# Performance work log

Measured on AMD Instinct MI355X. Metric: run time of the kernel, lower is better.

## Reference

```python
import jax, jax.numpy as jnp
import numpy as np

N = 100000
E = 3200000
K = 10
ALPHA = 0.1
EPS = 1e-5


def setup_inputs() -> dict:
    key = jax.random.key(0)
    ks = jax.random.split(key, 12)
    x = jax.random.normal(ks[0], (N, 512), dtype=jnp.float32)
    edge_index = jax.random.randint(ks[1], (2, E), 0, N, dtype=jnp.int32)
    w1 = jax.random.normal(ks[2], (128, 512), dtype=jnp.float32) * 0.02
    b1 = jnp.zeros((128,), jnp.float32)
    g1 = jnp.ones((128,), jnp.float32)
    be1 = jnp.zeros((128,), jnp.float32)
    m1 = jax.random.normal(ks[3], (128,), dtype=jnp.float32) * 0.1
    v1 = jax.random.uniform(ks[4], (128,), dtype=jnp.float32, minval=0.5, maxval=1.5)
    w2 = jax.random.normal(ks[5], (128, 128), dtype=jnp.float32) * 0.02
    b2 = jnp.zeros((128,), jnp.float32)
    g2 = jnp.ones((128,), jnp.float32)
    be2 = jnp.zeros((128,), jnp.float32)
    m2 = jax.random.normal(ks[6], (128,), dtype=jnp.float32) * 0.1
    v2 = jax.random.uniform(ks[7], (128,), dtype=jnp.float32, minval=0.5, maxval=1.5)
    w3 = jax.random.normal(ks[8], (3, 128), dtype=jnp.float32) * 0.02
    b3 = jnp.zeros((3,), jnp.float32)
    return dict(x=x, edge_index=edge_index, w1=w1, b1=b1, g1=g1, be1=be1, m1=m1, v1=v1,
                w2=w2, b2=b2, g2=g2, be2=be2, m2=m2, v2=v2, w3=w3, b3=b3)


def _bn(y, g, be, m, v):
    return (y - m) * jax.lax.rsqrt(v + EPS) * g + be


def reference(x, edge_index, w1, b1, g1, be1, m1, v1, w2, b2, g2, be2, m2, v2, w3, b3):
    # MLP (eval mode: BN uses running stats, dropout is identity)
    h = jax.nn.relu(_bn(x @ w1.T + b1, g1, be1, m1, v1))
    h = h + jax.nn.relu(_bn(h @ w2.T + b2, g2, be2, m2, v2))
    h = h @ w3.T + b3  # [N, 3]

    # APPNP propagation with GCN normalization + self-loops
    loop = jnp.arange(N, dtype=edge_index.dtype)
    src = jnp.concatenate([edge_index[0], loop])
    dst = jnp.concatenate([edge_index[1], loop])
    deg = jax.ops.segment_sum(jnp.ones_like(src, dtype=h.dtype), dst, num_segments=N)
    dinv = jnp.where(deg > 0, jax.lax.rsqrt(deg), 0.0)
    norm = dinv[src] * dinv[dst]  # [E+N]

    h0 = h
    z = h
    for _ in range(K):
        msg = z[src] * norm[:, None]
        z = jax.ops.segment_sum(msg, dst, num_segments=N)
        z = (1.0 - ALPHA) * z + ALPHA * h0
    return jax.nn.log_softmax(z, axis=1)
```

## Files before the change

kernel.cpp:

```cpp
#include <hip/hip_runtime.h>
#include <cstdint>
#include <cstddef>

#define N_NODES 100000
#define D_IN 512
#define ALPHA 0.1f
#define EPS_BN 1e-5f
#define M_TILE 128
#define BK 64

#define CBITS 8
#define CNODES 256
#define NCBIN 391
#define TILE 8192
#define EPT 32
#define BINCAP 9216

typedef float f32x4 __attribute__((ext_vector_type(4)));
typedef __bf16 bf16x8 __attribute__((ext_vector_type(8)));
typedef unsigned short u16x8 __attribute__((ext_vector_type(8)));
typedef unsigned short u16x4 __attribute__((ext_vector_type(4)));

__device__ __forceinline__ unsigned short f2bf(float f) {
  unsigned u = __float_as_uint(f);
  u += 0x7fffu + ((u >> 16) & 1u);
  return (unsigned short)(u >> 16);
}
__device__ __forceinline__ float bf2f(unsigned short h) {
  return __uint_as_float(((unsigned)h) << 16);
}

__global__ void k_prep(const float* __restrict__ w1, const float* __restrict__ b1,
                       const float* __restrict__ g1, const float* __restrict__ be1,
                       const float* __restrict__ m1, const float* __restrict__ v1,
                       const float* __restrict__ w2, const float* __restrict__ b2,
                       const float* __restrict__ g2, const float* __restrict__ be2,
                       const float* __restrict__ m2, const float* __restrict__ v2,
                       unsigned short* __restrict__ w1b, unsigned short* __restrict__ w2b,
                       float* __restrict__ bias1, float* __restrict__ bias2,
                       int* __restrict__ bincur) {
  int idx = blockIdx.x * 256 + threadIdx.x;
  if (idx < 65536) {
    int n = idx >> 9;
    float s = g1[n] * rsqrtf(v1[n] + EPS_BN);
    w1b[idx] = f2bf(w1[idx] * s);
  } else if (idx < 81920) {
    int i = idx - 65536;
    int n = i >> 7;
    float s = g2[n] * rsqrtf(v2[n] + EPS_BN);
    w2b[i] = f2bf(w2[i] * s);
  } else if (idx < 82048) {
    int c = idx - 81920;
    float s = g1[c] * rsqrtf(v1[c] + EPS_BN);
    bias1[c] = (b1[c] - m1[c]) * s + be1[c];
  } else if (idx < 82176) {
    int c = idx - 82048;
    float s = g2[c] * rsqrtf(v2[c] + EPS_BN);
    bias2[c] = (b2[c] - m2[c]) * s + be2[c];
  }
  int bi = idx - 82176;
  if (bi >= 0 && bi < NCBIN) bincur[bi] = 0;
}

__global__ void k_scan1(const int* __restrict__ deg, int* __restrict__ bsum) {
  __shared__ int red[256];
  int t = threadIdx.x;
  int i = blockIdx.x * 256 + t;
  red[t] = (i < N_NODES) ? deg[i] : 0;
  __syncthreads();
  for (int off = 128; off > 0; off >>= 1) {
    if (t < off) red[t] += red[t + off];
    __syncthreads();
  }
  if (t == 0) bsum[blockIdx.x] = red[0];
}

#define NB_SCAN 391
__global__ void k_scan2(int* __restrict__ bsum) {
  __shared__ int s[448];
  int t = threadIdx.x;
  for (int i = t; i < 448; i += 256) s[i] = (i < NB_SCAN) ? bsum[i] : 0;
  __syncthreads();
  if (t < 64) {
    int base = t * 7;
    int vals[7];
    int sum = 0;
#pragma unroll
    for (int j = 0; j < 7; ++j) { vals[j] = s[base + j]; sum += vals[j]; }
    int x = sum;
#pragma unroll
    for (int off = 1; off < 64; off <<= 1) {
      int y = __shfl_up(x, off, 64);
      if (t >= off) x += y;
    }
    int run = x - sum;
#pragma unroll
    for (int j = 0; j < 7; ++j) { int tmp = vals[j]; s[base + j] = run; run += tmp; }
  }
  __syncthreads();
  for (int i = t; i < NB_SCAN; i += 256) bsum[i] = s[i];
}

__global__ void k_scan3(const int* __restrict__ deg, const int* __restrict__ bsum,
                        int* __restrict__ row_start, float* __restrict__ dinv, int E) {
  __shared__ int sb[2][256];
  int t = threadIdx.x;
  int i = blockIdx.x * 256 + t;
  int d = (i < N_NODES) ? deg[i] : 0;
  sb[0][t] = d;
  __syncthreads();
  int cur = 0;
#pragma unroll
  for (int off = 1; off < 256; off <<= 1) {
    int val = sb[cur][t] + ((t >= off) ? sb[cur][t - off] : 0);
    sb[cur ^ 1][t] = val;
    __syncthreads();
    cur ^= 1;
  }
  int incl = sb[cur][t];
  int ex = incl - d;
  if (i < N_NODES) {
    int rs = bsum[blockIdx.x] + ex;
    row_start[i] = rs;
    dinv[i] = rsqrtf((float)(d + 1));
  }
  if (i == N_NODES) row_start[N_NODES] = E;
}

__global__ __launch_bounds__(256) void k_binA(const int* __restrict__ src,
                                              const int* __restrict__ dst, int E,
                                              int* __restrict__ bincur,
                                              unsigned* __restrict__ binned) {
  __shared__ unsigned stage[TILE];
  __shared__ int cnt[NCBIN];
  __shared__ int loff[NCBIN + 1];
  __shared__ int goff[NCBIN];
  __shared__ int sc[2][256];
  const int tid = threadIdx.x;

  for (int i = tid; i < NCBIN; i += 256) cnt[i] = 0;
  __syncthreads();

  const int e0 = blockIdx.x * TILE;
  const int n = min(TILE, E - e0);

  unsigned pk[EPT];
  int bp[EPT];
#pragma unroll
  for (int i = 0; i < EPT; ++i) {
    int o = i * 256 + tid;
    if (o < n) {
      int e = e0 + o;
      int d = dst[e];
      int s = src[e];
      int b = d >> CBITS;
      pk[i] = (unsigned)s | ((unsigned)(d & (CNODES - 1)) << 17);
      int p = atomicAdd(&cnt[b], 1);
      bp[i] = b | (p << 9);
    } else bp[i] = -1;
  }
  __syncthreads();

  int c0 = (2 * tid     < NCBIN) ? cnt[2 * tid]     : 0;
  int c1 = (2 * tid + 1 < NCBIN) ? cnt[2 * tid + 1] : 0;
  sc[0][tid] = c0 + c1;
  __syncthreads();
  int cur = 0;
#pragma unroll
  for (int off = 1; off < 256; off <<= 1) {
    sc[cur ^ 1][tid] = sc[cur][tid] + ((tid >= off) ? sc[cur][tid - off] : 0);
    __syncthreads();
    cur ^= 1;
  }
  int ex = sc[cur][tid] - (c0 + c1);
  if (2 * tid < NCBIN) loff[2 * tid] = ex;
  if (2 * tid + 1 < NCBIN) loff[2 * tid + 1] = ex + c0;
  if (tid == 255) loff[NCBIN] = sc[cur][255];
  __syncthreads();
  for (int i = tid; i < NCBIN; i += 256)
    if (cnt[i] > 0) goff[i] = atomicAdd(&bincur[i], cnt[i]);
  __syncthreads();

#pragma unroll
  for (int i = 0; i < EPT; ++i) {
    if (bp[i] >= 0) {
      int b = bp[i] & 511;
      int p = bp[i] >> 9;
      stage[loff[b] + p] = pk[i];
    }
  }
  __syncthreads();

  for (int i = tid; i < n; i += 256) {
    int lo = 0, hi = NCBIN;
    while (hi - lo > 1) { int mid = (lo + hi) >> 1; if (loff[mid] <= i) lo = mid; else hi = mid; }
    int b = lo;
    binned[(size_t)b * BINCAP + goff[b] + (i - loff[b])] = stage[i];
  }
}

__global__ __launch_bounds__(256) void k_binB1(const unsigned* __restrict__ binned,
                                               const int* __restrict__ bincur,
                                               int* __restrict__ deg) {
  __shared__ int lcnt[CNODES];
  int b = blockIdx.x;
  int t = threadIdx.x;
  lcnt[t] = 0;
  __syncthreads();
  int cnt = bincur[b];
  const unsigned* bp = binned + (size_t)b * BINCAP;
  for (int i = t; i < cnt; i += 256) {
    unsigned v = bp[i];
    atomicAdd(&lcnt[v >> 17], 1);
  }
  __syncthreads();
  int node = (b << CBITS) + t;
  if (node < N_NODES) deg[node] = lcnt[t];
}

__global__ __launch_bounds__(256) void k_binB2(const unsigned* __restrict__ binned,
                                               const int* __restrict__ bincur,
                                               const int* __restrict__ row_start,
                                               unsigned* __restrict__ csr_col) {
  __shared__ unsigned sortbuf[BINCAP];
  __shared__ int lcur[CNODES];
  int b = blockIdx.x;
  int t = threadIdx.x;
  int node0 = b << CBITS;
  int nodes = min(CNODES, N_NODES - node0);
  int rs0 = row_start[node0];
  if (t < nodes) lcur[t] = row_start[node0 + t] - rs0;
  __syncthreads();
  int cnt = bincur[b];
  const unsigned* bp = binned + (size_t)b * BINCAP;
  for (int i = t; i < cnt; i += 256) {
    unsigned v = bp[i];
    int p = atomicAdd(&lcur[v >> 17], 1);
    sortbuf[p] = v & 0x1FFFFu;
  }
  __syncthreads();
  for (int i = t; i < cnt; i += 256) csr_col[rs0 + i] = sortbuf[i];
}

__global__ __launch_bounds__(256, 2) void k_mlp(
    const float* __restrict__ x, const unsigned short* __restrict__ w1b,
    const unsigned short* __restrict__ w2b, const float* __restrict__ bias1,
    const float* __restrict__ bias2, const float* __restrict__ w3,
    const float* __restrict__ b3, const float* __restrict__ dinv,
    float4* __restrict__ h0, float4* __restrict__ zt) {
  __shared__ unsigned short arena[35840];
  __shared__ float lds_w3[384];
  unsigned short* lds_x = arena;
  unsigned short* lds_w = arena + 9216;
  unsigned short* lds_h = arena;
  unsigned short* lds_w2 = arena + 18432;

  const int tid = threadIdx.x;
  const int lane = tid & 63;
  const int wv = tid >> 6;
  const int fr = lane & 15;
  const int kq = (lane >> 4) * 8;
  const int rq = (lane >> 4) * 4;
  const int row0 = blockIdx.x * M_TILE;

  for (int i = tid; i < 384; i += 256) lds_w3[i] = w3[i];

#pragma unroll
  for (int it = 0; it < 8; ++it) {
    int idx = it * 256 + tid;
    int n = idx >> 4, c8 = idx & 15;
    uint4 v = *(const uint4*)(w2b + n * 128 + c8 * 8);
    *(uint4*)(lds_w2 + n * 136 + c8 * 8) = v;
  }

  f32x4 zero4 = {0.f, 0.f, 0.f, 0.f};
  f32x4 acc[2][8];
#pragma unroll
  for (int mt = 0; mt < 2; ++mt)
#pragma unroll
    for (int nt = 0; nt < 8; ++nt) acc[mt][nt] = zero4;

  for (int kb = 0; kb < D_IN; kb += BK) {
#pragma unroll
    for (int it = 0; it < 8; ++it) {
      int idx = it * 256 + tid;
      int r = idx >> 4, c4 = idx & 15;
      int gm = row0 + r;
      if (gm >= N_NODES) gm = N_NODES - 1;
      float4 v = *(const float4*)(x + (size_t)gm * D_IN + kb + c4 * 4);
      u16x4 o;
      o.x = f2bf(v.x); o.y = f2bf(v.y); o.z = f2bf(v.z); o.w = f2bf(v.w);
      *(u16x4*)(lds_x + r * 72 + c4 * 4) = o;
    }
#pragma unroll
    for (int it = 0; it < 4; ++it) {
      int idx = it * 256 + tid;
      int n = idx >> 3, c8 = idx & 7;
      uint4 v = *(const uint4*)(w1b + n * 512 + kb + c8 * 8);
      *(uint4*)(lds_w + n * 72 + c8 * 8) = v;
    }
    __syncthreads();
#pragma unroll
    for (int kk = 0; kk < BK; kk += 32) {
      bf16x8 a[2], b[8];
#pragma unroll
      for (int mt = 0; mt < 2; ++mt)
        a[mt] = __builtin_bit_cast(bf16x8, *(const u16x8*)(lds_x + (wv * 32 + mt * 16 + fr) * 72 + kk + kq));
#pragma unroll
      for (int nt = 0; nt < 8; ++nt)
        b[nt] = __builtin_bit_cast(bf16x8, *(const u16x8*)(lds_w + (nt * 16 + fr) * 72 + kk + kq));
#pragma unroll
      for (int mt = 0; mt < 2; ++mt)
#pragma unroll
        for (int nt = 0; nt < 8; ++nt)
          acc[mt][nt] = __builtin_amdgcn_mfma_f32_16x16x32_bf16(a[mt], b[nt], acc[mt][nt], 0, 0, 0);
    }
    __syncthreads();
  }

  float b1v[8], b2v[8];
#pragma unroll
  for (int nt = 0; nt < 8; ++nt) {
    b1v[nt] = bias1[nt * 16 + fr];
    b2v[nt] = bias2[nt * 16 + fr];
  }
  float hr[2][8][4];
#pragma unroll
  for (int mt = 0; mt < 2; ++mt)
#pragma unroll
    for (int nt = 0; nt < 8; ++nt)
#pragma unroll
      for (int r = 0; r < 4; ++r) {
        int rl = wv * 32 + mt * 16 + rq + r;
        int cl = nt * 16 + fr;
        float h = acc[mt][nt][r] + b1v[nt];
        h = h > 0.f ? h : 0.f;
        hr[mt][nt][r] = h;
        lds_h[rl * 136 + cl] = f2bf(h);
      }
  __syncthreads();

  f32x4 acc2[2][8];
#pragma unroll
  for (int mt = 0; mt < 2; ++mt)
#pragma unroll
    for (int nt = 0; nt < 8; ++nt) acc2[mt][nt] = zero4;
#pragma unroll
  for (int kk = 0; kk < 128; kk += 32) {
    bf16x8 a[2], b[8];
#pragma unroll
    for (int mt = 0; mt < 2; ++mt)
      a[mt] = __builtin_bit_cast(bf16x8, *(const u16x8*)(lds_h + (wv * 32 + mt * 16 + fr) * 136 + kk + kq));
#pragma unroll
    for (int nt = 0; nt < 8; ++nt)
      b[nt] = __builtin_bit_cast(bf16x8, *(const u16x8*)(lds_w2 + (nt * 16 + fr) * 136 + kk + kq));
#pragma unroll
    for (int mt = 0; mt < 2; ++mt)
#pragma unroll
      for (int nt = 0; nt < 8; ++nt)
        acc2[mt][nt] = __builtin_amdgcn_mfma_f32_16x16x32_bf16(a[mt], b[nt], acc2[mt][nt], 0, 0, 0);
  }
  __syncthreads();

#pragma unroll
  for (int mt = 0; mt < 2; ++mt)
#pragma unroll
    for (int nt = 0; nt < 8; ++nt)
#pragma unroll
      for (int r = 0; r < 4; ++r) {
        int rl = wv * 32 + mt * 16 + rq + r;
        int cl = nt * 16 + fr;
        float t2 = acc2[mt][nt][r] + b2v[nt];
        t2 = t2 > 0.f ? t2 : 0.f;
        lds_h[rl * 136 + cl] = f2bf(hr[mt][nt][r] + t2);
      }
  __syncthreads();

  if (tid < 128) {
    int m = tid;
    int gm = row0 + m;
    if (gm < N_NODES) {
      float a0 = 0.f, a1 = 0.f, a2 = 0.f;
#pragma unroll 8
      for (int c = 0; c < 128; ++c) {
        float hv = bf2f(lds_h[m * 136 + c]);
        a0 += hv * lds_w3[c];
        a1 += hv * lds_w3[128 + c];
        a2 += hv * lds_w3[256 + c];
      }
      float z0 = a0 + b3[0], z1 = a1 + b3[1], z2 = a2 + b3[2];
      float di = dinv[gm];
      h0[gm] = make_float4(z0, z1, z2, 0.f);
      zt[gm] = make_float4(di * z0, di * z1, di * z2, 0.f);
    }
  }
}

__global__ void k_iter(const float4* __restrict__ ztin, float4* __restrict__ ztout,
                       const int* __restrict__ row_start, const unsigned* __restrict__ csr_col,
                       const float* __restrict__ dinv, const float4* __restrict__ h0) {
  int i = blockIdx.x * 256 + threadIdx.x;
  if (i >= N_NODES) return;
  float4 self = ztin[i];
  float sx = self.x, sy = self.y, sz = self.z;
  int r0 = row_start[i], r1 = row_start[i + 1];
  int j = r0;
  for (; j + 1 < r1; j += 2) {
    int c0 = csr_col[j], c1 = csr_col[j + 1];
    float4 v0 = ztin[c0];
    float4 v1 = ztin[c1];
    sx += v0.x + v1.x; sy += v0.y + v1.y; sz += v0.z + v1.z;
  }
  if (j < r1) {
    float4 v = ztin[csr_col[j]];
    sx += v.x; sy += v.y; sz += v.z;
  }
  float di = dinv[i];
  float4 h = h0[i];
  float zx = (1.f - ALPHA) * di * sx + ALPHA * h.x;
  float zy = (1.f - ALPHA) * di * sy + ALPHA * h.y;
  float zz = (1.f - ALPHA) * di * sz + ALPHA * h.z;
  ztout[i] = make_float4(di * zx, di * zy, di * zz, 0.f);
}

__global__ void k_final(const float4* __restrict__ ztin,
                        const int* __restrict__ row_start, const unsigned* __restrict__ csr_col,
                        const float* __restrict__ dinv, const float4* __restrict__ h0,
                        float* __restrict__ out) {
  int i = blockIdx.x * 256 + threadIdx.x;
  if (i >= N_NODES) return;
  float4 self = ztin[i];
  float sx = self.x, sy = self.y, sz = self.z;
  int r0 = row_start[i], r1 = row_start[i + 1];
  int j = r0;
  for (; j + 1 < r1; j += 2) {
    int c0 = csr_col[j], c1 = csr_col[j + 1];
    float4 v0 = ztin[c0];
    float4 v1 = ztin[c1];
    sx += v0.x + v1.x; sy += v0.y + v1.y; sz += v0.z + v1.z;
  }
  if (j < r1) {
    float4 v = ztin[csr_col[j]];
    sx += v.x; sy += v.y; sz += v.z;
  }
  float di = dinv[i];
  float4 h = h0[i];
  float zx = (1.f - ALPHA) * di * sx + ALPHA * h.x;
  float zy = (1.f - ALPHA) * di * sy + ALPHA * h.y;
  float zz = (1.f - ALPHA) * di * sz + ALPHA * h.z;
  float mx = fmaxf(zx, fmaxf(zy, zz));
  float l = logf(expf(zx - mx) + expf(zy - mx) + expf(zz - mx));
  out[i * 3 + 0] = zx - mx - l;
  out[i * 3 + 1] = zy - mx - l;
  out[i * 3 + 2] = zz - mx - l;
}

extern "C" void kernel_launch(void* const* d_in, const int* in_sizes, int n_in,
                              void* d_out, int out_size, void* d_ws, size_t ws_size,
                              hipStream_t stream) {
  const float* x   = (const float*)d_in[0];
  const int*   ei  = (const int*)d_in[1];
  const float* w1  = (const float*)d_in[2];
  const float* b1  = (const float*)d_in[3];
  const float* g1  = (const float*)d_in[4];
  const float* be1 = (const float*)d_in[5];
  const float* m1  = (const float*)d_in[6];
  const float* v1  = (const float*)d_in[7];
  const float* w2  = (const float*)d_in[8];
  const float* b2  = (const float*)d_in[9];
  const float* g2  = (const float*)d_in[10];
  const float* be2 = (const float*)d_in[11];
  const float* m2  = (const float*)d_in[12];
  const float* v2  = (const float*)d_in[13];
  const float* w3  = (const float*)d_in[14];
  const float* b3  = (const float*)d_in[15];

  const int E = in_sizes[1] / 2;
  const int* srcA = ei;
  const int* dstA = ei + E;

  char* w = (char*)d_ws;
  size_t off = 0;
  auto alloc = [&](size_t bytes) -> void* {
    void* p = w + off;
    off = (off + bytes + 255) & ~(size_t)255;
    return p;
  };
  unsigned short* w1b   = (unsigned short*)alloc(65536 * 2);
  unsigned short* w2b   = (unsigned short*)alloc(16384 * 2);
  float* bias1          = (float*)alloc(128 * 4);
  float* bias2          = (float*)alloc(128 * 4);
  int*   deg            = (int*)alloc((size_t)N_NODES * 4);
  int*   row_start      = (int*)alloc(((size_t)N_NODES + 1) * 4);
  float* dinv           = (float*)alloc((size_t)N_NODES * 4);
  int*   bsum           = (int*)alloc(512 * 4);
  int*   bincur         = (int*)alloc((size_t)NCBIN * 4);
  float4* h0            = (float4*)alloc((size_t)N_NODES * 16);
  float4* ztA           = (float4*)alloc((size_t)N_NODES * 16);
  float4* ztB           = (float4*)alloc((size_t)N_NODES * 16);
  unsigned* csr_col     = (unsigned*)alloc((size_t)E * 4);
  unsigned* binned      = (unsigned*)alloc((size_t)NCBIN * BINCAP * 4);

  const int NB = (N_NODES + 255) / 256;
  const int NTILE = (E + TILE - 1) / TILE;

  k_prep<<<(82176 + NCBIN + 255) / 256, 256, 0, stream>>>(
      w1, b1, g1, be1, m1, v1, w2, b2, g2, be2, m2, v2, w1b, w2b, bias1, bias2, bincur);
  k_binA<<<NTILE, 256, 0, stream>>>(srcA, dstA, E, bincur, binned);
  k_binB1<<<NCBIN, 256, 0, stream>>>(binned, bincur, deg);
  k_scan1<<<NB, 256, 0, stream>>>(deg, bsum);
  k_scan2<<<1, 256, 0, stream>>>(bsum);
  k_scan3<<<NB, 256, 0, stream>>>(deg, bsum, row_start, dinv, E);
  k_binB2<<<NCBIN, 256, 0, stream>>>(binned, bincur, row_start, csr_col);
  k_mlp<<<(N_NODES + M_TILE - 1) / M_TILE, 256, 0, stream>>>(
      x, w1b, w2b, bias1, bias2, w3, b3, dinv, h0, ztA);

  const float4* zin = ztA;
  float4* zout = ztB;
  for (int k = 0; k < 9; ++k) {
    k_iter<<<NB, 256, 0, stream>>>(zin, zout, row_start, csr_col, dinv, h0);
    const float4* t = zout;
    zout = (float4*)zin;
    zin = t;
  }
  k_final<<<NB, 256, 0, stream>>>(zin, row_start, csr_col, dinv, h0, (float*)d_out);
}
```

Before: 677.7 us.

## Fuse APPNP iterations into persistent kernel with grid barrier and LDS-cached indices

Result: slower. 2.182 ms (+222.0%).

```diff
diff --git a/kernel.cpp b/kernel.cpp
--- a/kernel.cpp
+++ b/kernel.cpp
@@ -15,6 +15,10 @@
 #define TILE 8192
 #define EPT 32
 #define BINCAP 9216
+
+#define NPB 128
+#define NB2 782
+#define LCAP 4800
 
 typedef float f32x4 __attribute__((ext_vector_type(4)));
 typedef __bf16 bf16x8 __attribute__((ext_vector_type(8)));
@@ -38,8 +42,9 @@
                        const float* __restrict__ m2, const float* __restrict__ v2,
                        unsigned short* __restrict__ w1b, unsigned short* __restrict__ w2b,
                        float* __restrict__ bias1, float* __restrict__ bias2,
-                       int* __restrict__ bincur) {
+                       int* __restrict__ bincur, int* __restrict__ bar) {
   int idx = blockIdx.x * 256 + threadIdx.x;
+  if (idx == 0) bar[0] = 0;
   if (idx < 65536) {
     int n = idx >> 9;
     float s = g1[n] * rsqrtf(v1[n] + EPS_BN);
@@ -396,63 +401,104 @@
   }
 }
 
-__global__ void k_iter(const float4* __restrict__ ztin, float4* __restrict__ ztout,
-                       const int* __restrict__ row_start, const unsigned* __restrict__ csr_col,
-                       const float* __restrict__ dinv, const float4* __restrict__ h0) {
-  int i = blockIdx.x * 256 + threadIdx.x;
-  if (i >= N_NODES) return;
-  float4 self = ztin[i];
-  float sx = self.x, sy = self.y, sz = self.z;
-  int r0 = row_start[i], r1 = row_start[i + 1];
-  int j = r0;
-  for (; j + 1 < r1; j += 2) {
-    int c0 = csr_col[j], c1 = csr_col[j + 1];
-    float4 v0 = ztin[c0];
-    float4 v1 = ztin[c1];
-    sx += v0.x + v1.x; sy += v0.y + v1.y; sz += v0.z + v1.z;
-  }
-  if (j < r1) {
-    float4 v = ztin[csr_col[j]];
-    sx += v.x; sy += v.y; sz += v.z;
-  }
-  float di = dinv[i];
-  float4 h = h0[i];
-  float zx = (1.f - ALPHA) * di * sx + ALPHA * h.x;
-  float zy = (1.f - ALPHA) * di * sy + ALPHA * h.y;
-  float zz = (1.f - ALPHA) * di * sz + ALPHA * h.z;
-  ztout[i] = make_float4(di * zx, di * zy, di * zz, 0.f);
-}
-
-__global__ void k_final(const float4* __restrict__ ztin,
-                        const int* __restrict__ row_start, const unsigned* __restrict__ csr_col,
-                        const float* __restrict__ dinv, const float4* __restrict__ h0,
-                        float* __restrict__ out) {
-  int i = blockIdx.x * 256 + threadIdx.x;
-  if (i >= N_NODES) return;
-  float4 self = ztin[i];
-  float sx = self.x, sy = self.y, sz = self.z;
-  int r0 = row_start[i], r1 = row_start[i + 1];
-  int j = r0;
-  for (; j + 1 < r1; j += 2) {
-    int c0 = csr_col[j], c1 = csr_col[j + 1];
-    float4 v0 = ztin[c0];
-    float4 v1 = ztin[c1];
-    sx += v0.x + v1.x; sy += v0.y + v1.y; sz += v0.z + v1.z;
-  }
-  if (j < r1) {
-    float4 v = ztin[csr_col[j]];
-    sx += v.x; sy += v.y; sz += v.z;
-  }
-  float di = dinv[i];
-  float4 h = h0[i];
-  float zx = (1.f - ALPHA) * di * sx + ALPHA * h.x;
-  float zy = (1.f - ALPHA) * di * sy + ALPHA * h.y;
-  float zz = (1.f - ALPHA) * di * sz + ALPHA * h.z;
-  float mx = fmaxf(zx, fmaxf(zy, zz));
-  float l = logf(expf(zx - mx) + expf(zy - mx) + expf(zz - mx));
-  out[i * 3 + 0] = zx - mx - l;
-  out[i * 3 + 1] = zy - mx - l;
-  out[i * 3 + 2] = zz - mx - l;
+__global__ __launch_bounds__(256, 4) void k_prop(
+    float4* __restrict__ ztA, float4* __restrict__ ztB,
+    const int* __restrict__ row_start, const unsigned* __restrict__ csr_col,
+    const float* __restrict__ dinv, const float4* __restrict__ h0v,
+    float* __restrict__ out, int* __restrict__ bar) {
+  __shared__ unsigned lidx[LCAP];
+  __shared__ float psum[NPB][3];
+  __shared__ int s_r[2];
+  const int t = threadIdx.x;
+  const int half = t >> 7;
+  const int tn = t & 127;
+  const int node0 = blockIdx.x * NPB;
+  const int node = node0 + tn;
+  const bool valid = node < N_NODES;
+
+  if (t == 0) s_r[0] = row_start[node0];
+  if (t == 1) {
+    int hi = node0 + NPB;
+    if (hi > N_NODES) hi = N_NODES;
+    s_r[1] = row_start[hi];
+  }
+  __syncthreads();
+  const int rs0 = s_r[0];
+  int cnt = s_r[1] - rs0;
+  if (cnt > LCAP) cnt = LCAP;
+  for (int i = t; i < cnt; i += 256) lidx[i] = csr_col[rs0 + i];
+
+  int jb = 0, je = 0;
+  float h0x = 0.f, h0y = 0.f, h0z = 0.f, di = 0.f;
+  float sfx = 0.f, sfy = 0.f, sfz = 0.f;
+  if (valid) {
+    int r0 = row_start[node] - rs0;
+    int r1 = row_start[node + 1] - rs0;
+    int rm = (r0 + r1 + 1) >> 1;
+    jb = half ? rm : r0;
+    je = half ? r1 : rm;
+    if (half == 0) {
+      float4 h = h0v[node];
+      h0x = h.x; h0y = h.y; h0z = h.z;
+      di = dinv[node];
+      sfx = di * h0x; sfy = di * h0y; sfz = di * h0z;
+    }
+  }
+  __syncthreads();
+
+  for (int it = 0; it < 10; ++it) {
+    const float4* zin = (it & 1) ? (const float4*)ztB : (const float4*)ztA;
+    float4* zout = (it & 1) ? ztA : ztB;
+
+    float sx = 0.f, sy = 0.f, sz = 0.f;
+    int j = jb;
+    for (; j + 3 < je; j += 4) {
+      int c0 = lidx[j], c1 = lidx[j + 1], c2 = lidx[j + 2], c3 = lidx[j + 3];
+      float4 v0 = zin[c0];
+      float4 v1 = zin[c1];
+      float4 v2 = zin[c2];
+      float4 v3 = zin[c3];
+      sx += (v0.x + v1.x) + (v2.x + v3.x);
+      sy += (v0.y + v1.y) + (v2.y + v3.y);
+      sz += (v0.z + v1.z) + (v2.z + v3.z);
+    }
+    for (; j < je; ++j) {
+      float4 v = zin[lidx[j]];
+      sx += v.x; sy += v.y; sz += v.z;
+    }
+    if (half) { psum[tn][0] = sx; psum[tn][1] = sy; psum[tn][2] = sz; }
+    __syncthreads();
+    if (half == 0 && valid) {
+      sx += psum[tn][0] + sfx;
+      sy += psum[tn][1] + sfy;
+      sz += psum[tn][2] + sfz;
+      float zx = (1.f - ALPHA) * di * sx + ALPHA * h0x;
+      float zy = (1.f - ALPHA) * di * sy + ALPHA * h0y;
+      float zz = (1.f - ALPHA) * di * sz + ALPHA * h0z;
+      if (it < 9) {
+        sfx = di * zx; sfy = di * zy; sfz = di * zz;
+        zout[node] = make_float4(sfx, sfy, sfz, 0.f);
+      } else {
+        float mx = fmaxf(zx, fmaxf(zy, zz));
+        float l = logf(expf(zx - mx) + expf(zy - mx) + expf(zz - mx));
+        out[node * 3 + 0] = zx - mx - l;
+        out[node * 3 + 1] = zy - mx - l;
+        out[node * 3 + 2] = zz - mx - l;
+      }
+    }
+    if (it < 9) {
+      __threadfence();
+      __syncthreads();
+      if (t == 0) {
+        __hip_atomic_fetch_add(bar, 1, __ATOMIC_ACQ_REL, __HIP_MEMORY_SCOPE_AGENT);
+        const int target = (it + 1) * NB2;
+        while (__hip_atomic_load(bar, __ATOMIC_RELAXED, __HIP_MEMORY_SCOPE_AGENT) < target)
+          __builtin_amdgcn_s_sleep(2);
+      }
+      __syncthreads();
+      __threadfence();
+    }
+  }
 }
 
 extern "C" void kernel_launch(void* const* d_in, const int* in_sizes, int n_in,
@@ -495,6 +541,7 @@
   float* dinv           = (float*)alloc((size_t)N_NODES * 4);
   int*   bsum           = (int*)alloc(512 * 4);
   int*   bincur         = (int*)alloc((size_t)NCBIN * 4);
+  int*   bar            = (int*)alloc(256);
   float4* h0            = (float4*)alloc((size_t)N_NODES * 16);
   float4* ztA           = (float4*)alloc((size_t)N_NODES * 16);
   float4* ztB           = (float4*)alloc((size_t)N_NODES * 16);
@@ -505,7 +552,7 @@
   const int NTILE = (E + TILE - 1) / TILE;
 
   k_prep<<<(82176 + NCBIN + 255) / 256, 256, 0, stream>>>(
-      w1, b1, g1, be1, m1, v1, w2, b2, g2, be2, m2, v2, w1b, w2b, bias1, bias2, bincur);
+      w1, b1, g1, be1, m1, v1, w2, b2, g2, be2, m2, v2, w1b, w2b, bias1, bias2, bincur, bar);
   k_binA<<<NTILE, 256, 0, stream>>>(srcA, dstA, E, bincur, binned);
   k_binB1<<<NCBIN, 256, 0, stream>>>(binned, bincur, deg);
   k_scan1<<<NB, 256, 0, stream>>>(deg, bsum);
@@ -514,14 +561,5 @@
   k_binB2<<<NCBIN, 256, 0, stream>>>(binned, bincur, row_start, csr_col);
   k_mlp<<<(N_NODES + M_TILE - 1) / M_TILE, 256, 0, stream>>>(
       x, w1b, w2b, bias1, bias2, w3, b3, dinv, h0, ztA);
-
-  const float4* zin = ztA;
-  float4* zout = ztB;
-  for (int k = 0; k < 9; ++k) {
-    k_iter<<<NB, 256, 0, stream>>>(zin, zout, row_start, csr_col, dinv, h0);
-    const float4* t = zout;
-    zout = (float4*)zin;
-    zin = t;
-  }
-  k_final<<<NB, 256, 0, stream>>>(zin, row_start, csr_col, dinv, h0, (float*)d_out);
-}
+  k_prop<<<NB2, 256, 0, stream>>>(ztA, ztB, row_start, csr_col, dinv, h0, (float*)d_out, bar);
+}
```
